# Kernel tuning notes

Hardware: AMD Instinct MI355X
Metric: run time of the kernel (lower is better)

## Reference

```python
import jax, jax.numpy as jnp
import numpy as np

EPS = 1e-5  # torch InstanceNorm2d default eps


def _patches(x):
    """3x3 patches with padding 1. [B,C,H,W] -> [B,C,9,H,W]."""
    B, C, H, W = x.shape
    xp = jnp.pad(x, ((0, 0), (0, 0), (1, 1), (1, 1)))
    cols = [xp[:, :, dy:dy + H, dx:dx + W] for dy in range(3) for dx in range(3)]
    return jnp.stack(cols, axis=2)


def _instance_norm(x):
    # per-(batch, channel) normalization over spatial dims, biased variance, no affine
    mu = jnp.mean(x, axis=(2, 3), keepdims=True)
    var = jnp.mean((x - mu) ** 2, axis=(2, 3), keepdims=True)
    return (x - mu) * jax.lax.rsqrt(var + EPS)


def setup_inputs() -> dict:
    key = jax.random.key(0)
    ks = jax.random.split(key, 6)
    B, Cin, Cout, H, W = 4, 128, 64, 128, 128
    feat = jax.random.normal(ks[0], (B, Cin, H, W), dtype=jnp.float32)
    guide = jax.random.normal(ks[1], (B, Cin, H, W), dtype=jnp.float32)
    # PacConv2d weight/bias (Cin -> Cin, 3x3)
    pac_w = jax.random.normal(ks[2], (Cin, Cin, 3, 3), dtype=jnp.float32) * 0.02
    pac_b = jax.random.normal(ks[3], (Cin,), dtype=jnp.float32) * 0.02
    # decoding Conv2d weight/bias (Cin -> Cout, 3x3)
    conv_w = jax.random.normal(ks[4], (Cout, Cin, 3, 3), dtype=jnp.float32) * 0.02
    conv_b = jax.random.normal(ks[5], (Cout,), dtype=jnp.float32) * 0.02
    return {"feat": feat, "guide": guide, "pac_w": pac_w, "pac_b": pac_b,
            "conv_w": conv_w, "conv_b": conv_b}


def reference(feat, guide, pac_w, pac_b, conv_w, conv_b):
    B, C, H, W = feat.shape
    O = pac_w.shape[0]
    # --- PacConv2d: pixel-adaptive Gaussian kernel from the guide ---
    g = _patches(guide)                                   # [B,Cg,9,H,W]
    diff2 = jnp.sum((g - guide[:, :, None]) ** 2, axis=1, keepdims=True)
    kern = jnp.exp(-0.5 * diff2)                          # [B,1,9,H,W]
    f = _patches(feat) * kern                             # [B,C,9,H,W]
    pac = jnp.einsum('bckhw,ock->bohw', f, pac_w.reshape(O, C, 9))
    pac = pac + pac_b[None, :, None, None]
    # --- InstanceNorm + ReLU ---
    x = jax.nn.relu(_instance_norm(pac))
    # --- decoding: Conv2d 3x3 + InstanceNorm + ReLU ---
    y = jax.lax.conv_general_dilated(x, conv_w, window_strides=(1, 1),
                                     padding=((1, 1), (1, 1)))
    y = y + conv_b[None, :, None, None]
    return jax.nn.relu(_instance_norm(y))
```

## Files before the change

### kernel.cpp

```cpp
#include <hip/hip_runtime.h>

#define H 128
#define W 128
#define HW 16384
#define CIN 128
#define COUT 64
#define BATCH 4
#define EPS 1e-5f
#define PY 130
#define PX 132

#define FB_OFF    0
#define XNB_OFF   4392960
#define KPART_OFF XNB_OFF
#define KERN_OFF  (XNB_OFF + 4392960)
#define WT_OFF    (KERN_OFF + 589824)
#define CT_OFF    (WT_OFF + 73728)
#define STATS_OFF (CT_OFF + 36864)
#define SUM1   (STATS_OFF)
#define SUMSQ1 (STATS_OFF + 512)
#define SUM2   (STATS_OFF + 1024)
#define SUMSQ2 (STATS_OFF + 1280)
#define SCALE1 (STATS_OFF + 1536)
#define SHIFT1 (STATS_OFF + 2048)
#define SCALE2 (STATS_OFF + 2560)
#define SHIFT2 (STATS_OFF + 2816)

typedef float f32x4 __attribute__((ext_vector_type(4)));
typedef short bf16x8 __attribute__((ext_vector_type(8)));
typedef short bf16x4 __attribute__((ext_vector_type(4)));
#define MFMA16 __builtin_amdgcn_mfma_f32_16x16x32_bf16

__device__ __forceinline__ unsigned short f2b(float f) {
  union { float f; unsigned u; } un; un.f = f;
  unsigned r = un.u + 0x7FFF + ((un.u >> 16) & 1);
  return (unsigned short)(r >> 16);
}
__device__ __forceinline__ float b2f(unsigned short u) {
  union { unsigned u; float f; } x; x.u = ((unsigned)u) << 16; return x.f;
}
__device__ __forceinline__ void load_lds16(const void* g, void* l) {
  __builtin_amdgcn_global_load_lds(
      (const __attribute__((address_space(1))) unsigned int*)g,
      (__attribute__((address_space(3))) unsigned int*)l, 16, 0, 0);
}

__device__ __forceinline__ void decode_wg(int bid, int& b, int& y, int& x0) {
  int wgid = (bid & 7) * 128 + (bid >> 3);
  b = wgid >> 8;
  int rem = wgid & 255;
  y = rem >> 1;
  x0 = (rem & 1) << 6;
}

__global__ __launch_bounds__(256) void zero_pads(float* __restrict__ ws) {
  int id = blockIdx.x * 256 + threadIdx.x;
  if (id >= 4 * 776 * 16) return;
  int chunk = id & 15; int rest = id >> 4;
  int px = rest % 776; int b = rest / 776;
  int row, xx;
  if (px < 264) { row = (px < 132) ? 0 : 129; xx = px % 132; }
  else { int q = px - 264; row = 1 + (q >> 2); int m = q & 3; xx = m ? 128 + m : 0; }
  unsigned short* base = (unsigned short*)(ws + FB_OFF);
  bf16x8 z = {0, 0, 0, 0, 0, 0, 0, 0};
  *(bf16x8*)(base + ((b * PY + row) * PX + xx) * 128 + chunk * 8) = z;
}

__global__ __launch_bounds__(256) void transpose_feat(const float* __restrict__ feat,
                                                      float* __restrict__ ws) {
  __shared__ __align__(16) char T[128 * 256];
  int b = blockIdx.x >> 7, y = blockIdx.x & 127;
  int t = threadIdx.x;
  int x = t & 127, ch = t >> 7;
  const float* fp = feat + ((b * CIN) << 14) + (y << 7) + x;
#pragma unroll 8
  for (int cc = 0; cc < 64; ++cc) {
    int c = ch * 64 + cc;
    float v = fp[c << 14];
    int byte = (x << 8) + (c << 1);
    byte ^= (x & 7) << 4;
    *(unsigned short*)(T + byte) = f2b(v);
  }
  __syncthreads();
  unsigned short* fb = (unsigned short*)(ws + FB_OFF);
#pragma unroll
  for (int it = 0; it < 8; ++it) {
    int flat = it * 256 + t;
    int px = flat >> 4, j = flat & 15;
    int byte = (px << 8) + (j << 4);
    byte ^= (px & 7) << 4;
    bf16x8 v = *(bf16x8*)(T + byte);
    *(bf16x8*)(fb + ((b * PY + y + 1) * PX + px + 1) * 128 + j * 8) = v;
  }
}

__global__ __launch_bounds__(256) void kern_part(const float* __restrict__ guide,
                                                 float* __restrict__ ws) {
  int p = blockIdx.x * 256 + threadIdx.x;
  int cs = blockIdx.y;
  int b = p >> 14;
  int pix = p & (HW - 1);
  int y = pix >> 7, x = pix & (W - 1);
  float acc[9];
#pragma unroll
  for (int k = 0; k < 9; ++k) acc[k] = 0.f;
  const float* gb = guide + ((b * CIN + cs * 32) << 14);
  for (int c = 0; c < 32; ++c) {
    const float* gc = gb + (c << 14);
    float g0 = gc[pix];
#pragma unroll
    for (int dy = -1; dy <= 1; ++dy) {
#pragma unroll
      for (int dx = -1; dx <= 1; ++dx) {
        int yy = y + dy, xx = x + dx;
        bool ok = ((unsigned)yy < (unsigned)H) && ((unsigned)xx < (unsigned)W);
        int yc = min(max(yy, 0), H - 1);
        int xc = min(max(xx, 0), W - 1);
        float g = gc[yc * W + xc];
        g = ok ? g : 0.f;
        float d = g - g0;
        acc[(dy + 1) * 3 + (dx + 1)] += d * d;
      }
    }
  }
  float* kp = ws + KPART_OFF;
#pragma unroll
  for (int k = 0; k < 9; ++k)
    kp[(((cs * BATCH + b) * 9 + k) << 14) + pix] = acc[k];
}

__global__ __launch_bounds__(256) void expk(float* __restrict__ ws) {
  int i = blockIdx.x * 256 + threadIdx.x;
  const float4* kp = reinterpret_cast<const float4*>(ws + KPART_OFF);
  float4 a = kp[i], b = kp[i + 147456], c = kp[i + 2 * 147456], d = kp[i + 3 * 147456];
  float4 o;
  o.x = __expf(-0.5f * (a.x + b.x + c.x + d.x));
  o.y = __expf(-0.5f * (a.y + b.y + c.y + d.y));
  o.z = __expf(-0.5f * (a.z + b.z + c.z + d.z));
  o.w = __expf(-0.5f * (a.w + b.w + c.w + d.w));
  reinterpret_cast<float4*>(ws + KERN_OFF)[i] = o;
}

__global__ __launch_bounds__(256) void prep_w(const float* __restrict__ pw,
                                              const float* __restrict__ cw,
                                              float* __restrict__ ws) {
  int t = blockIdx.x * 256 + threadIdx.x;
  unsigned short* Wtu = (unsigned short*)(ws + WT_OFF);
  unsigned short* Ctu = (unsigned short*)(ws + CT_OFF);
  if (t < 147456) {
    int k = t >> 14, rem = t & 16383, o = rem >> 7, c = rem & 127;
    Wtu[t] = f2b(pw[(o * CIN + c) * 9 + k]);
  } else {
    int u = t - 147456;
    int k = u >> 13, rem = u & 8191, o = rem >> 7, c = rem & 127;
    Ctu[u] = f2b(cw[(o * CIN + c) * 9 + k]);
  }
}

__device__ __forceinline__ void stage_tile(const unsigned short* __restrict__ src_base,
                                           char* Fs, int b, int y, int x0, int t) {
  int lane = t & 63, w = t >> 6;
  int j = lane & 15, pl = lane >> 4;
#pragma unroll
  for (int q = 0; q < 12; ++q) {
    int m = w * 12 + q;
    int r = m >> 4, pblk = m & 15;
    int p = 1 + pblk * 4 + pl;
    int jx = (j & 8) | ((j & 7) ^ (p & 7));
    const unsigned short* src = src_base + (((b * PY + y + r) * PX + x0 + p) << 7) + jx * 8;
    char* dst = Fs + ((r * 66 + 1 + pblk * 4) << 8);
    load_lds16(src, dst);
  }
  if (t < 96) {
    int r = t >> 5, side = (t >> 4) & 1, jj = t & 15;
    int p = side ? 65 : 0;
    int jx = (jj & 8) | ((jj & 7) ^ (p & 7));
    const unsigned short* src = src_base + (((b * PY + y + r) * PX + x0 + p) << 7) + jx * 8;
    bf16x8 v = *(const bf16x8*)src;
    *(bf16x8*)(Fs + ((r * 66 + p) << 8) + jj * 16) = v;
  }
}

__device__ __forceinline__ void stage_fused(const unsigned short* __restrict__ src_base,
                                            char* Fs, const float* __restrict__ sc,
                                            const float* __restrict__ sh,
                                            int b, int y, int x0, int t) {
  int lane = t & 63, w = t >> 6;
  int j = lane & 15, pl = lane >> 4;
#pragma unroll
  for (int q = 0; q < 12; ++q) {
    int m = w * 12 + q;
    int r = m >> 4, pblk = m & 15;
    int p = 1 + pblk * 4 + pl;
    int jx = (j & 8) | ((j & 7) ^ (p & 7));
    int yy = y + r, xx = x0 + p;
    bf16x8 v = *(const bf16x8*)(src_base + (((b * PY + yy) * PX + xx) << 7) + jx * 8);
    bool pad = (yy == 0) | (yy == PY - 1) | (xx == 0) | (xx >= PX - 3);
    f32x4 s0 = *(const f32x4*)(sc + jx * 8), s1 = *(const f32x4*)(sc + jx * 8 + 4);
    f32x4 h0 = *(const f32x4*)(sh + jx * 8), h1 = *(const f32x4*)(sh + jx * 8 + 4);
    bf16x8 o;
#pragma unroll
    for (int e = 0; e < 4; ++e) {
      float a0 = fmaxf(fmaf(b2f((unsigned short)v[e]), s0[e], h0[e]), 0.f);
      float a1 = fmaxf(fmaf(b2f((unsigned short)v[e + 4]), s1[e], h1[e]), 0.f);
      o[e] = (short)f2b(pad ? 0.f : a0);
      o[e + 4] = (short)f2b(pad ? 0.f : a1);
    }
    *(bf16x8*)(Fs + ((r * 66 + p) << 8) + j * 16) = o;
  }
  if (t < 96) {
    int r = t >> 5, side = (t >> 4) & 1, jj = t & 15;
    int p = side ? 65 : 0;
    int jx = (jj & 8) | ((jj & 7) ^ (p & 7));
    int yy = y + r, xx = x0 + p;
    bf16x8 v = *(const bf16x8*)(src_base + (((b * PY + yy) * PX + xx) << 7) + jx * 8);
    bool pad = (yy == 0) | (yy == PY - 1) | (xx == 0) | (xx >= PX - 3);
    f32x4 s0 = *(const f32x4*)(sc + jx * 8), s1 = *(const f32x4*)(sc + jx * 8 + 4);
    f32x4 h0 = *(const f32x4*)(sh + jx * 8), h1 = *(const f32x4*)(sh + jx * 8 + 4);
    bf16x8 o;
#pragma unroll
    for (int e = 0; e < 4; ++e) {
      float a0 = fmaxf(fmaf(b2f((unsigned short)v[e]), s0[e], h0[e]), 0.f);
      float a1 = fmaxf(fmaf(b2f((unsigned short)v[e + 4]), s1[e], h1[e]), 0.f);
      o[e] = (short)f2b(pad ? 0.f : a0);
      o[e + 4] = (short)f2b(pad ? 0.f : a1);
    }
    *(bf16x8*)(Fs + ((r * 66 + p) << 8) + jj * 16) = o;
  }
}

__global__ __launch_bounds__(256, 2) void pac_mfma(float* __restrict__ ws) {
  __shared__ __align__(16) char Fs[3 * 66 * 256];
  int b, y, x0;
  decode_wg(blockIdx.x, b, y, x0);
  const int t = threadIdx.x;
  const unsigned short* Wtu = (const unsigned short*)(ws + WT_OFF);
  const unsigned short* fb = (const unsigned short*)(ws + FB_OFF);
  unsigned short* xnb = (unsigned short*)(ws + XNB_OFF);
  const int lane = t & 63, l15 = lane & 15, lg = lane >> 4;
  const int o0 = (t >> 6) * 32;

  const unsigned short* Wbase = Wtu + (o0 + l15) * 128 + lg * 8;
  const float* kernb = ws + KERN_OFF + ((b * 9) << 14) + (y << 7) + x0 + l15;

  bf16x8 wa[3][8];
  float kr[3][4];
#pragma unroll
  for (int pk = 0; pk < 2; ++pk) {
#pragma unroll
    for (int ks = 0; ks < 4; ++ks) {
      wa[pk][ks * 2 + 0] = *(const bf16x8*)(Wbase + pk * 16384 + ks * 32);
      wa[pk][ks * 2 + 1] = *(const bf16x8*)(Wbase + pk * 16384 + 2048 + ks * 32);
    }
#pragma unroll
    for (int pt = 0; pt < 4; ++pt) kr[pk][pt] = kernb[(pk << 14) + pt * 16];
  }

  stage_tile(fb, Fs, b, y, x0, t);
  __syncthreads();

  const f32x4 vzero = {0.f, 0.f, 0.f, 0.f};
  f32x4 pacc0[4], pacc1[4];
#pragma unroll
  for (int pt = 0; pt < 4; ++pt) { pacc0[pt] = vzero; pacc1[pt] = vzero; }

#pragma unroll
  for (int k = 0; k < 9; ++k) {
    const int dy = k / 3, dxi = k % 3;
    const int cur = k % 3;
    if (k + 2 <= 8) {
      const int nb = (k + 2) % 3;
#pragma unroll
      for (int ks = 0; ks < 4; ++ks) {
        wa[nb][ks * 2 + 0] = *(const bf16x8*)(Wbase + (k + 2) * 16384 + ks * 32);
        wa[nb][ks * 2 + 1] = *(const bf16x8*)(Wbase + (k + 2) * 16384 + 2048 + ks * 32);
      }
#pragma unroll
      for (int pt = 0; pt < 4; ++pt) kr[nb][pt] = kernb[((k + 2) << 14) + pt * 16];
    }
    f32x4 z0[4], z1[4];
#pragma unroll
    for (int ks = 0; ks < 4; ++ks) {
#pragma unroll
      for (int pt = 0; pt < 4; ++pt) {
        int p = dxi + pt * 16 + l15;
        int byte = ((dy * 66 + p) << 8) + ks * 64 + lg * 16;
        byte ^= (p & 7) << 4;
        bf16x8 bv = *(const bf16x8*)(Fs + byte);
        z0[pt] = MFMA16(wa[cur][ks * 2 + 0], bv, ks ? z0[pt] : vzero, 0, 0, 0);
        z1[pt] = MFMA16(wa[cur][ks * 2 + 1], bv, ks ? z1[pt] : vzero, 0, 0, 0);
      }
    }
#pragma unroll
    for (int pt = 0; pt < 4; ++pt) {
      float kvv = kr[cur][pt];
#pragma unroll
      for (int i = 0; i < 4; ++i) {
        pacc0[pt][i] = fmaf(kvv, z0[pt][i], pacc0[pt][i]);
        pacc1[pt][i] = fmaf(kvv, z1[pt][i], pacc1[pt][i]);
      }
    }
  }

  float* sum1 = ws + SUM1;
  float* sumsq1 = ws + SUMSQ1;
#pragma unroll
  for (int pt = 0; pt < 4; ++pt) {
    int px = x0 + pt * 16 + l15;
    int base = ((b * PY + y + 1) * PX + px + 1) * 128;
    bf16x4 vA, vB;
#pragma unroll
    for (int i = 0; i < 4; ++i) { vA[i] = (short)f2b(pacc0[pt][i]); vB[i] = (short)f2b(pacc1[pt][i]); }
    *(bf16x4*)(xnb + base + o0 + lg * 4) = vA;
    *(bf16x4*)(xnb + base + o0 + 16 + lg * 4) = vB;
  }
#pragma unroll
  for (int half = 0; half < 2; ++half) {
#pragma unroll
    for (int i = 0; i < 4; ++i) {
      float s = 0.f, sq = 0.f;
#pragma unroll
      for (int pt = 0; pt < 4; ++pt) {
        float v = half ? pacc1[pt][i] : pacc0[pt][i];
        s += v; sq += v * v;
      }
#pragma unroll
      for (int m = 1; m < 16; m <<= 1) {
        s += __shfl_xor(s, m);
        sq += __shfl_xor(sq, m);
      }
      if (l15 == 0) {
        int o = o0 + half * 16 + lg * 4 + i;
        atomicAdd(&sum1[b * CIN + o], s);
        atomicAdd(&sumsq1[b * CIN + o], sq);
      }
    }
  }
}

__global__ void stats_kernel(float* __restrict__ ws, int sumoff, int sqoff,
                             int scoff, int shoff, int n, float invN) {
  int i = blockIdx.x * blockDim.x + threadIdx.x;
  if (i >= n) return;
  float mu = ws[sumoff + i] * invN;
  float var = ws[sqoff + i] * invN - mu * mu;
  var = fmaxf(var, 0.f);
  float rs = rsqrtf(var + EPS);
  ws[scoff + i] = rs;
  ws[shoff + i] = -mu * rs;
}

__global__ __launch_bounds__(256, 3) void conv_mfma(float* __restrict__ ws,
                                                    float* __restrict__ out) {
  __shared__ __align__(16) char Xs[3 * 66 * 256];
  int b, y, x0;
  decode_wg(blockIdx.x, b, y, x0);
  const int t = threadIdx.x;
  const unsigned short* Ctu = (const unsigned short*)(ws + CT_OFF);
  const unsigned short* xnb = (const unsigned short*)(ws + XNB_OFF);
  const float* sc1 = ws + SCALE1 + b * CIN;
  const float* sh1 = ws + SHIFT1 + b * CIN;
  const int lane = t & 63, l15 = lane & 15, lg = lane >> 4;
  const int o0 = (t >> 6) * 16;

  const unsigned short* Cbase = Ctu + (o0 + l15) * 128 + lg * 8;

  bf16x8 wa[3][4];
#pragma unroll
  for (int pk = 0; pk < 2; ++pk)
#pragma unroll
    for (int ks = 0; ks < 4; ++ks)
      wa[pk][ks] = *(const bf16x8*)(Cbase + pk * 8192 + ks * 32);

  stage_fused(xnb, Xs, sc1, sh1, b, y, x0, t);
  __syncthreads();

  const f32x4 vzero = {0.f, 0.f, 0.f, 0.f};
  f32x4 acc[4];
#pragma unroll
  for (int pt = 0; pt < 4; ++pt) acc[pt] = vzero;

#pragma unroll
  for (int k = 0; k < 9; ++k) {
    const int dy = k / 3, dxi = k % 3;
    const int cur = k % 3;
    if (k + 2 <= 8) {
      const int nb = (k + 2) % 3;
#pragma unroll
      for (int ks = 0; ks < 4; ++ks)
        wa[nb][ks] = *(const bf16x8*)(Cbase + (k + 2) * 8192 + ks * 32);
    }
#pragma unroll
    for (int ks = 0; ks < 4; ++ks) {
#pragma unroll
      for (int pt = 0; pt < 4; ++pt) {
        int p = dxi + pt * 16 + l15;
        int byte = ((dy * 66 + p) << 8) + ks * 64 + lg * 16;
        byte ^= (p & 7) << 4;
        bf16x8 bv = *(const bf16x8*)(Xs + byte);
        acc[pt] = MFMA16(wa[cur][ks], bv, acc[pt], 0, 0, 0);
      }
    }
  }

  float* sum2 = ws + SUM2;
  float* sumsq2 = ws + SUMSQ2;
#pragma unroll
  for (int pt = 0; pt < 4; ++pt) {
#pragma unroll
    for (int i = 0; i < 4; ++i) {
      int o = o0 + lg * 4 + i;
      int px = x0 + pt * 16 + l15;
      out[((b * COUT + o) << 14) + (y << 7) + px] = acc[pt][i];
    }
  }
#pragma unroll
  for (int i = 0; i < 4; ++i) {
    float s = 0.f, sq = 0.f;
#pragma unroll
    for (int pt = 0; pt < 4; ++pt) { float v = acc[pt][i]; s += v; sq += v * v; }
#pragma unroll
    for (int m = 1; m < 16; m <<= 1) {
      s += __shfl_xor(s, m);
      sq += __shfl_xor(sq, m);
    }
    if (l15 == 0) {
      int o = o0 + lg * 4 + i;
      atomicAdd(&sum2[b * COUT + o], s);
      atomicAdd(&sumsq2[b * COUT + o], sq);
    }
  }
}

__global__ __launch_bounds__(256) void norm_kernel(float* __restrict__ out,
                                                   const float* __restrict__ ws) {
  int i = blockIdx.x * 256 + threadIdx.x;
  int bc = (i * 4) >> 14;
  float sc = ws[SCALE2 + bc];
  float sh = ws[SHIFT2 + bc];
  float4 v = reinterpret_cast<float4*>(out)[i];
  v.x = fmaxf(fmaf(v.x, sc, sh), 0.f);
  v.y = fmaxf(fmaf(v.y, sc, sh), 0.f);
  v.z = fmaxf(fmaf(v.z, sc, sh), 0.f);
  v.w = fmaxf(fmaf(v.w, sc, sh), 0.f);
  reinterpret_cast<float4*>(out)[i] = v;
}

extern "C" void kernel_launch(void* const* d_in, const int* in_sizes, int n_in,
                              void* d_out, int out_size, void* d_ws, size_t ws_size,
                              hipStream_t stream) {
  const float* feat = (const float*)d_in[0];
  const float* guide = (const float*)d_in[1];
  const float* pac_w = (const float*)d_in[2];
  const float* conv_w = (const float*)d_in[4];
  float* ws = (float*)d_ws;
  float* out = (float*)d_out;

  hipMemsetAsync(ws + STATS_OFF, 0, 1536 * sizeof(float), stream);

  prep_w<<<dim3(864), 256, 0, stream>>>(pac_w, conv_w, ws);
  zero_pads<<<dim3(194), 256, 0, stream>>>(ws);
  transpose_feat<<<dim3(512), 256, 0, stream>>>(feat, ws);
  kern_part<<<dim3(256, 4), 256, 0, stream>>>(guide, ws);
  expk<<<dim3(576), 256, 0, stream>>>(ws);
  pac_mfma<<<dim3(1024), 256, 0, stream>>>(ws);
  stats_kernel<<<dim3(2), 256, 0, stream>>>(ws, SUM1, SUMSQ1, SCALE1, SHIFT1,
                                            BATCH * CIN, 1.f / HW);
  conv_mfma<<<dim3(1024), 256, 0, stream>>>(ws, out);
  stats_kernel<<<dim3(1), 256, 0, stream>>>(ws, SUM2, SUMSQ2, SCALE2, SHIFT2,
                                            BATCH * COUT, 1.f / HW);
  norm_kernel<<<dim3(BATCH * COUT * HW / 1024), 256, 0, stream>>>(out, ws);
}
```

Baseline: 160.7 us.

## Merge four prep kernels into one launch and raise wave priority around MFMA loops

```diff
diff --git a/kernel.cpp b/kernel.cpp
--- a/kernel.cpp
+++ b/kernel.cpp
@@ -53,80 +53,97 @@
   x0 = (rem & 1) << 6;
 }
 
-__global__ __launch_bounds__(256) void zero_pads(float* __restrict__ ws) {
-  int id = blockIdx.x * 256 + threadIdx.x;
-  if (id >= 4 * 776 * 16) return;
-  int chunk = id & 15; int rest = id >> 4;
-  int px = rest % 776; int b = rest / 776;
-  int row, xx;
-  if (px < 264) { row = (px < 132) ? 0 : 129; xx = px % 132; }
-  else { int q = px - 264; row = 1 + (q >> 2); int m = q & 3; xx = m ? 128 + m : 0; }
-  unsigned short* base = (unsigned short*)(ws + FB_OFF);
-  bf16x8 z = {0, 0, 0, 0, 0, 0, 0, 0};
-  *(bf16x8*)(base + ((b * PY + row) * PX + xx) * 128 + chunk * 8) = z;
-}
-
-__global__ __launch_bounds__(256) void transpose_feat(const float* __restrict__ feat,
-                                                      float* __restrict__ ws) {
+__global__ __launch_bounds__(256) void prep_all(const float* __restrict__ feat,
+                                                const float* __restrict__ guide,
+                                                const float* __restrict__ pw,
+                                                const float* __restrict__ cw,
+                                                float* __restrict__ ws) {
   __shared__ __align__(16) char T[128 * 256];
-  int b = blockIdx.x >> 7, y = blockIdx.x & 127;
-  int t = threadIdx.x;
-  int x = t & 127, ch = t >> 7;
-  const float* fp = feat + ((b * CIN) << 14) + (y << 7) + x;
+  const int bid = blockIdx.x;
+  const int t = threadIdx.x;
+
+  if (bid < 512) {
+    int b = bid >> 7, y = bid & 127;
+    int x = t & 127, ch = t >> 7;
+    const float* fp = feat + ((b * CIN) << 14) + (y << 7) + x;
 #pragma unroll 8
-  for (int cc = 0; cc < 64; ++cc) {
-    int c = ch * 64 + cc;
-    float v = fp[c << 14];
-    int byte = (x << 8) + (c << 1);
-    byte ^= (x & 7) << 4;
-    *(unsigned short*)(T + byte) = f2b(v);
-  }
-  __syncthreads();
-  unsigned short* fb = (unsigned short*)(ws + FB_OFF);
-#pragma unroll
-  for (int it = 0; it < 8; ++it) {
-    int flat = it * 256 + t;
-    int px = flat >> 4, j = flat & 15;
-    int byte = (px << 8) + (j << 4);
-    byte ^= (px & 7) << 4;
-    bf16x8 v = *(bf16x8*)(T + byte);
-    *(bf16x8*)(fb + ((b * PY + y + 1) * PX + px + 1) * 128 + j * 8) = v;
-  }
-}
-
-__global__ __launch_bounds__(256) void kern_part(const float* __restrict__ guide,
-                                                 float* __restrict__ ws) {
-  int p = blockIdx.x * 256 + threadIdx.x;
-  int cs = blockIdx.y;
-  int b = p >> 14;
-  int pix = p & (HW - 1);
-  int y = pix >> 7, x = pix & (W - 1);
-  float acc[9];
-#pragma unroll
-  for (int k = 0; k < 9; ++k) acc[k] = 0.f;
-  const float* gb = guide + ((b * CIN + cs * 32) << 14);
-  for (int c = 0; c < 32; ++c) {
-    const float* gc = gb + (c << 14);
-    float g0 = gc[pix];
-#pragma unroll
-    for (int dy = -1; dy <= 1; ++dy) {
-#pragma unroll
-      for (int dx = -1; dx <= 1; ++dx) {
-        int yy = y + dy, xx = x + dx;
-        bool ok = ((unsigned)yy < (unsigned)H) && ((unsigned)xx < (unsigned)W);
-        int yc = min(max(yy, 0), H - 1);
-        int xc = min(max(xx, 0), W - 1);
-        float g = gc[yc * W + xc];
-        g = ok ? g : 0.f;
-        float d = g - g0;
-        acc[(dy + 1) * 3 + (dx + 1)] += d * d;
-      }
-    }
-  }
-  float* kp = ws + KPART_OFF;
-#pragma unroll
-  for (int k = 0; k < 9; ++k)
-    kp[(((cs * BATCH + b) * 9 + k) << 14) + pix] = acc[k];
+    for (int cc = 0; cc < 64; ++cc) {
+      int c = ch * 64 + cc;
+      float v = fp[c << 14];
+      int byte = (x << 8) + (c << 1);
+      byte ^= (x & 7) << 4;
+      *(unsigned short*)(T + byte) = f2b(v);
+    }
+    __syncthreads();
+    unsigned short* fb = (unsigned short*)(ws + FB_OFF);
+#pragma unroll
+    for (int it = 0; it < 8; ++it) {
+      int flat = it * 256 + t;
+      int px = flat >> 4, j = flat & 15;
+      int byte = (px << 8) + (j << 4);
+      byte ^= (px & 7) << 4;
+      bf16x8 v = *(bf16x8*)(T + byte);
+      *(bf16x8*)(fb + ((b * PY + y + 1) * PX + px + 1) * 128 + j * 8) = v;
+    }
+  } else if (bid < 706) {
+    int id = (bid - 512) * 256 + t;
+    if (id < 4 * 776 * 16) {
+      int chunk = id & 15; int rest = id >> 4;
+      int px = rest % 776; int b = rest / 776;
+      int row, xx;
+      if (px < 264) { row = (px < 132) ? 0 : 129; xx = px % 132; }
+      else { int q = px - 264; row = 1 + (q >> 2); int m = q & 3; xx = m ? 128 + m : 0; }
+      unsigned short* base = (unsigned short*)(ws + FB_OFF);
+      bf16x8 z = {0, 0, 0, 0, 0, 0, 0, 0};
+      *(bf16x8*)(base + ((b * PY + row) * PX + xx) * 128 + chunk * 8) = z;
+    }
+  } else if (bid < 1570) {
+    int tg = (bid - 706) * 256 + t;
+    unsigned short* Wtu = (unsigned short*)(ws + WT_OFF);
+    unsigned short* Ctu = (unsigned short*)(ws + CT_OFF);
+    if (tg < 147456) {
+      int k = tg >> 14, rem = tg & 16383, o = rem >> 7, c = rem & 127;
+      Wtu[tg] = f2b(pw[(o * CIN + c) * 9 + k]);
+    } else {
+      int u = tg - 147456;
+      int k = u >> 13, rem = u & 8191, o = rem >> 7, c = rem & 127;
+      Ctu[u] = f2b(cw[(o * CIN + c) * 9 + k]);
+    }
+  } else {
+    int rel = bid - 1570;
+    int cs = rel >> 8;
+    int p = (rel & 255) * 256 + t;
+    int b = p >> 14;
+    int pix = p & (HW - 1);
+    int y = pix >> 7, x = pix & (W - 1);
+    float acc[9];
+#pragma unroll
+    for (int k = 0; k < 9; ++k) acc[k] = 0.f;
+    const float* gb = guide + ((b * CIN + cs * 32) << 14);
+#pragma unroll 4
+    for (int c = 0; c < 32; ++c) {
+      const float* gc = gb + (c << 14);
+      float g0 = gc[pix];
+#pragma unroll
+      for (int dy = -1; dy <= 1; ++dy) {
+#pragma unroll
+        for (int dx = -1; dx <= 1; ++dx) {
+          int yy = y + dy, xx = x + dx;
+          bool ok = ((unsigned)yy < (unsigned)H) && ((unsigned)xx < (unsigned)W);
+          int yc = min(max(yy, 0), H - 1);
+          int xc = min(max(xx, 0), W - 1);
+          float g = gc[yc * W + xc];
+          g = ok ? g : 0.f;
+          float d = g - g0;
+          acc[(dy + 1) * 3 + (dx + 1)] += d * d;
+        }
+      }
+    }
+    float* kp = ws + KPART_OFF;
+#pragma unroll
+    for (int k = 0; k < 9; ++k)
+      kp[(((cs * BATCH + b) * 9 + k) << 14) + pix] = acc[k];
+  }
 }
 
 __global__ __launch_bounds__(256) void expk(float* __restrict__ ws) {
@@ -139,22 +156,6 @@
   o.z = __expf(-0.5f * (a.z + b.z + c.z + d.z));
   o.w = __expf(-0.5f * (a.w + b.w + c.w + d.w));
   reinterpret_cast<float4*>(ws + KERN_OFF)[i] = o;
-}
-
-__global__ __launch_bounds__(256) void prep_w(const float* __restrict__ pw,
-                                              const float* __restrict__ cw,
-                                              float* __restrict__ ws) {
-  int t = blockIdx.x * 256 + threadIdx.x;
-  unsigned short* Wtu = (unsigned short*)(ws + WT_OFF);
-  unsigned short* Ctu = (unsigned short*)(ws + CT_OFF);
-  if (t < 147456) {
-    int k = t >> 14, rem = t & 16383, o = rem >> 7, c = rem & 127;
-    Wtu[t] = f2b(pw[(o * CIN + c) * 9 + k]);
-  } else {
-    int u = t - 147456;
-    int k = u >> 13, rem = u & 8191, o = rem >> 7, c = rem & 127;
-    Ctu[u] = f2b(cw[(o * CIN + c) * 9 + k]);
-  }
 }
 
 __device__ __forceinline__ void stage_tile(const unsigned short* __restrict__ src_base,
@@ -279,6 +280,7 @@
       for (int pt = 0; pt < 4; ++pt) kr[nb][pt] = kernb[((k + 2) << 14) + pt * 16];
     }
     f32x4 z0[4], z1[4];
+    __builtin_amdgcn_s_setprio(1);
 #pragma unroll
     for (int ks = 0; ks < 4; ++ks) {
 #pragma unroll
@@ -291,6 +293,7 @@
         z1[pt] = MFMA16(wa[cur][ks * 2 + 1], bv, ks ? z1[pt] : vzero, 0, 0, 0);
       }
     }
+    __builtin_amdgcn_s_setprio(0);
 #pragma unroll
     for (int pt = 0; pt < 4; ++pt) {
       float kvv = kr[cur][pt];
@@ -390,6 +393,7 @@
       for (int ks = 0; ks < 4; ++ks)
         wa[nb][ks] = *(const bf16x8*)(Cbase + (k + 2) * 8192 + ks * 32);
     }
+    __builtin_amdgcn_s_setprio(1);
 #pragma unroll
     for (int ks = 0; ks < 4; ++ks) {
 #pragma unroll
@@ -401,6 +405,7 @@
         acc[pt] = MFMA16(wa[cur][ks], bv, acc[pt], 0, 0, 0);
       }
     }
+    __builtin_amdgcn_s_setprio(0);
   }
 
   float* sum2 = ws + SUM2;
@@ -458,10 +463,7 @@
 
   hipMemsetAsync(ws + STATS_OFF, 0, 1536 * sizeof(float), stream);
 
-  prep_w<<<dim3(864), 256, 0, stream>>>(pac_w, conv_w, ws);
-  zero_pads<<<dim3(194), 256, 0, stream>>>(ws);
-  transpose_feat<<<dim3(512), 256, 0, stream>>>(feat, ws);
-  kern_part<<<dim3(256, 4), 256, 0, stream>>>(guide, ws);
+  prep_all<<<dim3(2594), 256, 0, stream>>>(feat, guide, pac_w, conv_w, ws);
   expk<<<dim3(576), 256, 0, stream>>>(ws);
   pac_mfma<<<dim3(1024), 256, 0, stream>>>(ws);
   stats_kernel<<<dim3(2), 256, 0, stream>>>(ws, SUM1, SUMSQ1, SCALE1, SHIFT1,
```

Measured after the change: 157.4 us. -2.1%, faster.
